# Optimization experiments

Hardware: AMD Instinct MI355X
Metric: run time of the kernel (lower is better)

The kernel has to match this reference:

```python
import jax, jax.numpy as jnp
import numpy as np

P_FACTOR = 3.0
EPS = 1e-12  # matches torch F.normalize clamp_min eps


def _normalize(x):
    # L2-normalize along the feature (last) axis, like F.normalize(x, dim=1) on 2D
    n = jnp.sqrt(jnp.sum(x * x, axis=-1, keepdims=True))
    return x / jnp.maximum(n, EPS)


def setup_inputs() -> dict:
    key = jax.random.key(0)
    ks = jax.random.split(key, 7)
    N, M, F, E = 8192, 16384, 768, 512
    X = jax.random.normal(ks[0], (N, F), dtype=jnp.float32)
    D = jax.random.normal(ks[1], (M, F), dtype=jnp.float32)
    r = jax.random.uniform(ks[2], (M, 1), dtype=jnp.float32)
    g_w = jax.random.normal(ks[3], (E, F), dtype=jnp.float32) * (1.0 / np.sqrt(F))
    g_b = jax.random.normal(ks[4], (E,), dtype=jnp.float32) * 0.01
    h_w = jax.random.normal(ks[5], (1, 1), dtype=jnp.float32)
    h_b = jax.random.normal(ks[6], (1,), dtype=jnp.float32) * 0.01
    return {"X": X, "D": D, "r": r, "g_w": g_w, "g_b": g_b, "h_w": h_w, "h_b": h_b}


def reference(X, D, r, g_w, g_b, h_w, h_b):
    # r = r * 2 - 1  (map [0,1] correctness labels to [-1,1])
    r2 = r * 2.0 - 1.0
    # g: shared linear embedding of queries and exemplars
    Xg = X @ g_w.T + g_b          # [N, E]
    Dg = D @ g_w.T + g_b          # [M, E]
    # Minerva: cosine similarity
    a = _normalize(Xg) @ _normalize(Dg).T   # [N, M]
    # power-sign activation: |a|^p * sign(a)
    a = jnp.power(jnp.abs(a), P_FACTOR) * jnp.sign(a)
    # echo = weighted sum of exemplar labels
    echo = a @ r2                 # [N, 1]
    # h: Linear(1,1) then sigmoid
    out = jax.nn.sigmoid(echo @ h_w.T + h_b)  # [N, 1]
    return out
```

## Files before the change

kernel.cpp:

```cpp
#include <hip/hip_runtime.h>
#include <stdint.h>

#define F_DIM 768
#define E_DIM 512

typedef __attribute__((ext_vector_type(4))) float f32x4;
typedef __attribute__((ext_vector_type(8))) __bf16 bf16x8;

__device__ __forceinline__ uint16_t f2bf(float f) {
  uint32_t u = __builtin_bit_cast(uint32_t, f);
  return (uint16_t)((u + 0x7FFFu + ((u >> 16) & 1u)) >> 16);
}

#define GLOAD_LDS16(g, l) __builtin_amdgcn_global_load_lds(                 \
    (const __attribute__((address_space(1))) void*)(g),                     \
    (__attribute__((address_space(3))) void*)(l), 16, 0, 0)

__global__ __launch_bounds__(256) void embed_gemm(
    const float* __restrict__ src, const float* __restrict__ gw,
    const float* __restrict__ gb, uint16_t* __restrict__ out) {
  __shared__ uint4 smem4[2048];
  char* smc = (char*)smem4;
  const int t = threadIdx.x;
  const int l = t & 63, w = t >> 6, wm = w >> 1, wn = w & 1;
  const int bx = blockIdx.x, by = blockIdx.y;
  const int g = l >> 4, x7 = l & 7;

  f32x4 acc[4][4];
#pragma unroll
  for (int a_ = 0; a_ < 4; ++a_)
#pragma unroll
    for (int b_ = 0; b_ < 4; ++b_) acc[a_][b_] = (f32x4){0.f, 0.f, 0.f, 0.f};

  const int rr0 = t >> 3;
  const int ss  = t & 7;

  for (int kk = 0; kk < F_DIM; kk += 64) {
    __syncthreads();
#pragma unroll
    for (int c = 0; c < 4; ++c) {
      const int rr = c * 32 + rr0;
      const int wb = rr * 128 + ((ss ^ (rr & 7)) << 4);
      {
        const float* p = src + (size_t)(bx * 128 + rr) * F_DIM + kk + ss * 8;
        float4 lo = *(const float4*)p;
        float4 hi = *(const float4*)(p + 4);
        uint4 pk;
        pk.x = f2bf(lo.x) | ((uint32_t)f2bf(lo.y) << 16);
        pk.y = f2bf(lo.z) | ((uint32_t)f2bf(lo.w) << 16);
        pk.z = f2bf(hi.x) | ((uint32_t)f2bf(hi.y) << 16);
        pk.w = f2bf(hi.z) | ((uint32_t)f2bf(hi.w) << 16);
        *(uint4*)(smc + wb) = pk;
      }
      {
        const float* p = gw + (size_t)(by * 128 + rr) * F_DIM + kk + ss * 8;
        float4 lo = *(const float4*)p;
        float4 hi = *(const float4*)(p + 4);
        uint4 pk;
        pk.x = f2bf(lo.x) | ((uint32_t)f2bf(lo.y) << 16);
        pk.y = f2bf(lo.z) | ((uint32_t)f2bf(lo.w) << 16);
        pk.z = f2bf(hi.x) | ((uint32_t)f2bf(hi.y) << 16);
        pk.w = f2bf(hi.z) | ((uint32_t)f2bf(hi.w) << 16);
        *(uint4*)(smc + 16384 + wb) = pk;
      }
    }
    __syncthreads();
#pragma unroll
    for (int ks = 0; ks < 2; ++ks) {
      const int slotoff = ((ks * 4 + g) ^ x7) << 4;
      bf16x8 af[4], bfr[4];
#pragma unroll
      for (int fm = 0; fm < 4; ++fm)
        af[fm] = *(const bf16x8*)(smc + (wm * 64 + fm * 16 + (l & 15)) * 128 + slotoff);
#pragma unroll
      for (int fn = 0; fn < 4; ++fn)
        bfr[fn] = *(const bf16x8*)(smc + 16384 + (wn * 64 + fn * 16 + (l & 15)) * 128 + slotoff);
#pragma unroll
      for (int fm = 0; fm < 4; ++fm)
#pragma unroll
        for (int fn = 0; fn < 4; ++fn)
          acc[fm][fn] = __builtin_amdgcn_mfma_f32_16x16x32_bf16(
              af[fm], bfr[fn], acc[fm][fn], 0, 0, 0);
    }
  }

  const int colb = by * 128 + wn * 64;
#pragma unroll
  for (int fn = 0; fn < 4; ++fn) {
    const int col = colb + fn * 16 + (l & 15);
    const float bias = gb[col];
#pragma unroll
    for (int fm = 0; fm < 4; ++fm) {
      const int rowb = bx * 128 + wm * 64 + fm * 16 + g * 4;
#pragma unroll
      for (int v = 0; v < 4; ++v)
        out[(size_t)(rowb + v) * E_DIM + col] = f2bf(acc[fm][fn][v] + bias);
    }
  }
}

__global__ __launch_bounds__(256) void l2norm_rows(uint16_t* __restrict__ eg) {
  const int row = blockIdx.x * 4 + (threadIdx.x >> 6);
  const int l = threadIdx.x & 63;
  uint16_t* p = eg + (size_t)row * E_DIM + l * 8;
  uint4 v = *(const uint4*)p;
  uint32_t wd[4] = {v.x, v.y, v.z, v.w};
  float f[8];
#pragma unroll
  for (int i = 0; i < 4; ++i) {
    f[2 * i]     = __builtin_bit_cast(float, (wd[i] & 0xFFFFu) << 16);
    f[2 * i + 1] = __builtin_bit_cast(float, wd[i] & 0xFFFF0000u);
  }
  float s = 0.f;
#pragma unroll
  for (int i = 0; i < 8; ++i) s += f[i] * f[i];
#pragma unroll
  for (int m = 1; m < 64; m <<= 1) s += __shfl_xor(s, m);
  const float inv = 1.0f / fmaxf(sqrtf(s), 1e-12f);
  uint4 o;
  o.x = f2bf(f[0] * inv) | ((uint32_t)f2bf(f[1] * inv) << 16);
  o.y = f2bf(f[2] * inv) | ((uint32_t)f2bf(f[3] * inv) << 16);
  o.z = f2bf(f[4] * inv) | ((uint32_t)f2bf(f[5] * inv) << 16);
  o.w = f2bf(f[6] * inv) | ((uint32_t)f2bf(f[7] * inv) << 16);
  *(uint4*)p = o;
}

__global__ __launch_bounds__(512, 2) void minerva_main256(
    const uint16_t* __restrict__ Xn, const uint16_t* __restrict__ Dn,
    const float* __restrict__ rin, float* __restrict__ echo) {
  extern __shared__ __align__(16) char smem[];
  const int t_ = threadIdx.x;
  const int l = t_ & 63, w = t_ >> 6;
  const int wm = w >> 2, wn = w & 3;
  const int bx = blockIdx.x, by = blockIdx.y;
  const int g = l >> 4, x7 = l & 7, l15 = l & 15;

  f32x4 acc[8][4];
#pragma unroll
  for (int a_ = 0; a_ < 8; ++a_)
#pragma unroll
    for (int b_ = 0; b_ < 4; ++b_) acc[a_][b_] = (f32x4){0.f, 0.f, 0.f, 0.f};

  const int rr = t_ >> 3, ss = t_ & 7;
  const int s0 = ss ^ (rr & 7);
  const uint16_t* gA = Xn + (size_t)(bx * 256 + rr) * E_DIM + s0 * 8;
  const uint16_t* gB = Dn + (size_t)(by * 256 + rr) * E_DIM + s0 * 8;
  char* ldsDst = smem + t_ * 16;

#define STG_A(CUR, KK, I) GLOAD_LDS16(gA + (size_t)(I) * 64 * E_DIM + (KK), \
                                      ldsDst + (CUR) * 32768 + (I) * 8192)
#define STG_B(CUR, KK, I) GLOAD_LDS16(gB + (size_t)(I) * 64 * E_DIM + (KK), \
                                      ldsDst + 65536 + (CUR) * 32768 + (I) * 8192)

#define PHASE(FM0, KS, READ_B, GL, LAST)                                       \
  {                                                                            \
    const int so = (((KS) * 4 + g) ^ x7) << 4;                                 \
    bf16x8 af[4];                                                              \
    _Pragma("unroll") for (int i_ = 0; i_ < 4; ++i_)                           \
        af[i_] = *(const bf16x8*)(bufA +                                       \
                  (wm * 128 + ((FM0) + i_) * 16 + l15) * 128 + so);            \
    if (READ_B) {                                                              \
      _Pragma("unroll") for (int j_ = 0; j_ < 4; ++j_)                         \
          bfr[j_] = *(const bf16x8*)(bufB +                                    \
                    (wn * 64 + j_ * 16 + l15) * 128 + so);                     \
    }                                                                          \
    GL;                                                                        \
    __builtin_amdgcn_s_barrier();                                              \
    __builtin_amdgcn_s_setprio(1);                                             \
    _Pragma("unroll") for (int i_ = 0; i_ < 4; ++i_)                           \
        _Pragma("unroll") for (int j_ = 0; j_ < 4; ++j_)                       \
            acc[(FM0) + i_][j_] = __builtin_amdgcn_mfma_f32_16x16x32_bf16(     \
                af[i_], bfr[j_], acc[(FM0) + i_][j_], 0, 0, 0);                \
    __builtin_amdgcn_s_setprio(0);                                             \
    if (LAST) asm volatile("s_waitcnt vmcnt(0)" ::: "memory");                 \
    __builtin_amdgcn_s_barrier();                                              \
  }

#define TILE(KKN, CUR, PF)                                                     \
  {                                                                            \
    char* bufA = smem + (CUR) * 32768;                                         \
    char* bufB = smem + 65536 + (CUR) * 32768;                                 \
    bf16x8 bfr[4];                                                             \
    PHASE(0, 0, 1, if (PF) { STG_A(1 - (CUR), KKN, 0); STG_A(1 - (CUR), KKN, 1); }, 0) \
    PHASE(4, 0, 0, if (PF) { STG_A(1 - (CUR), KKN, 2); STG_A(1 - (CUR), KKN, 3); }, 0) \
    PHASE(0, 1, 1, if (PF) { STG_B(1 - (CUR), KKN, 0); STG_B(1 - (CUR), KKN, 1); }, 0) \
    PHASE(4, 1, 0, if (PF) { STG_B(1 - (CUR), KKN, 2); STG_B(1 - (CUR), KKN, 3); }, 1) \
  }

  STG_A(0, 0, 0); STG_A(0, 0, 1); STG_A(0, 0, 2); STG_A(0, 0, 3);
  STG_B(0, 0, 0); STG_B(0, 0, 1); STG_B(0, 0, 2); STG_B(0, 0, 3);
  asm volatile("s_waitcnt vmcnt(0)" ::: "memory");
  __builtin_amdgcn_s_barrier();

  for (int t2 = 0; t2 < 8; t2 += 2) {
    TILE((t2 + 1) * 64, 0, 1);
    const int pf2 = (t2 < 6);
    TILE((t2 + 2) * 64, 1, pf2);
  }

  const int jb = by * 256 + wn * 64;
  float r2[4];
#pragma unroll
  for (int fn = 0; fn < 4; ++fn)
    r2[fn] = rin[jb + fn * 16 + l15] * 2.0f - 1.0f;
  const int rowb = bx * 256 + wm * 128;
#pragma unroll
  for (int fm = 0; fm < 8; ++fm) {
#pragma unroll
    for (int v = 0; v < 4; ++v) {
      float sum = 0.f;
#pragma unroll
      for (int fn = 0; fn < 4; ++fn) {
        const float a = acc[fm][fn][v];
        sum += a * a * a * r2[fn];
      }
      sum += __shfl_xor(sum, 1);
      sum += __shfl_xor(sum, 2);
      sum += __shfl_xor(sum, 4);
      sum += __shfl_xor(sum, 8);
      if (l15 == 0)
        atomicAdd(&echo[rowb + fm * 16 + g * 4 + v], sum);
    }
  }
#undef STG_A
#undef STG_B
#undef PHASE
#undef TILE
}

__global__ __launch_bounds__(256) void head_sigmoid(
    const float* __restrict__ echo, const float* __restrict__ hw,
    const float* __restrict__ hb, float* __restrict__ out, int n) {
  const int i = blockIdx.x * 256 + threadIdx.x;
  if (i < n) {
    const float e = echo[i] * hw[0] + hb[0];
    out[i] = 1.0f / (1.0f + __expf(-e));
  }
}

extern "C" void kernel_launch(void* const* d_in, const int* in_sizes, int n_in,
                              void* d_out, int out_size, void* d_ws, size_t ws_size,
                              hipStream_t stream) {
  const float* X  = (const float*)d_in[0];
  const float* D  = (const float*)d_in[1];
  const float* r  = (const float*)d_in[2];
  const float* gw = (const float*)d_in[3];
  const float* gb = (const float*)d_in[4];
  const float* hw = (const float*)d_in[5];
  const float* hb = (const float*)d_in[6];
  float* out = (float*)d_out;
  const int N = in_sizes[0] / F_DIM;
  const int M = in_sizes[1] / F_DIM;

  uint16_t* Xn = (uint16_t*)d_ws;
  uint16_t* Dn = Xn + (size_t)N * E_DIM;
  float* echo = (float*)((char*)d_ws + (size_t)(N + M) * E_DIM * 2);

  hipMemsetAsync(echo, 0, (size_t)N * sizeof(float), stream);

  (void)hipFuncSetAttribute((const void*)minerva_main256,
                            hipFuncAttributeMaxDynamicSharedMemorySize, 131072);

  dim3 blk(256);
  embed_gemm<<<dim3(N / 128, E_DIM / 128), blk, 0, stream>>>(X, gw, gb, Xn);
  embed_gemm<<<dim3(M / 128, E_DIM / 128), blk, 0, stream>>>(D, gw, gb, Dn);
  l2norm_rows<<<(N + M) / 4, blk, 0, stream>>>(Xn);
  minerva_main256<<<dim3(N / 256, M / 256), dim3(512), 131072, stream>>>(Xn, Dn, r, echo);
  head_sigmoid<<<(N + 255) / 256, blk, 0, stream>>>(echo, hw, hb, out, N);
}
```

Before: 330.5 us.

## Pre-convert inputs to bf16, async-load embed GEMM, defer normalization to epilogue

Converts X, D and g_w to bf16 in separate passes into one concatenated buffer. The embedding GEMM then runs as a single launch that streams tiles straight into LDS with global_load_lds. This replaces the per-tile fp32 loading and conversion that was repeated for every output column block. The L2 normalization pass now computes only inverse row norms, and these are folded into the cosine-cube epilogue as ix^3 and id^3 factors instead of rewriting normalized embeddings. This adds extra passes over the input data, hardcodes the problem sizes, and runs the similarity GEMM on unnormalized bf16 values.

Result: slower. 370.5 us (+12.1%).

```diff
diff --git a/kernel.cpp b/kernel.cpp
--- a/kernel.cpp
+++ b/kernel.cpp
@@ -3,6 +3,9 @@
 
 #define F_DIM 768
 #define E_DIM 512
+#define N_ROWS 8192
+#define M_ROWS 16384
+#define T_ROWS (N_ROWS + M_ROWS)
 
 typedef __attribute__((ext_vector_type(4))) float f32x4;
 typedef __attribute__((ext_vector_type(8))) __bf16 bf16x8;
@@ -16,15 +19,31 @@
     (const __attribute__((address_space(1))) void*)(g),                     \
     (__attribute__((address_space(3))) void*)(l), 16, 0, 0)
 
-__global__ __launch_bounds__(256) void embed_gemm(
-    const float* __restrict__ src, const float* __restrict__ gw,
+__global__ __launch_bounds__(256) void cvt_f32_bf16(
+    const float* __restrict__ src, uint16_t* __restrict__ dst, int n8) {
+  int i = blockIdx.x * 256 + threadIdx.x;
+  const int stride = gridDim.x * 256;
+  for (; i < n8; i += stride) {
+    const float4 lo = *(const float4*)(src + (size_t)i * 8);
+    const float4 hi = *(const float4*)(src + (size_t)i * 8 + 4);
+    uint4 pk;
+    pk.x = f2bf(lo.x) | ((uint32_t)f2bf(lo.y) << 16);
+    pk.y = f2bf(lo.z) | ((uint32_t)f2bf(lo.w) << 16);
+    pk.z = f2bf(hi.x) | ((uint32_t)f2bf(hi.y) << 16);
+    pk.w = f2bf(hi.z) | ((uint32_t)f2bf(hi.w) << 16);
+    *(uint4*)(dst + (size_t)i * 8) = pk;
+  }
+}
+
+__global__ __launch_bounds__(256) void embed_gemm_bf(
+    const uint16_t* __restrict__ cat, const uint16_t* __restrict__ gwb,
     const float* __restrict__ gb, uint16_t* __restrict__ out) {
   __shared__ uint4 smem4[2048];
   char* smc = (char*)smem4;
   const int t = threadIdx.x;
   const int l = t & 63, w = t >> 6, wm = w >> 1, wn = w & 1;
   const int bx = blockIdx.x, by = blockIdx.y;
-  const int g = l >> 4, x7 = l & 7;
+  const int g = l >> 4, x7 = l & 7, l15 = l & 15;
 
   f32x4 acc[4][4];
 #pragma unroll
@@ -32,37 +51,19 @@
 #pragma unroll
     for (int b_ = 0; b_ < 4; ++b_) acc[a_][b_] = (f32x4){0.f, 0.f, 0.f, 0.f};
 
-  const int rr0 = t >> 3;
-  const int ss  = t & 7;
+  const int rr0 = t >> 3, ss = t & 7;
+  const int s0 = ss ^ (rr0 & 7);
+  const uint16_t* gA = cat + (size_t)(bx * 128 + rr0) * F_DIM + s0 * 8;
+  const uint16_t* gB = gwb + (size_t)(by * 128 + rr0) * F_DIM + s0 * 8;
+  char* ldsA = smc + t * 16;
+  char* ldsB = smc + 16384 + t * 16;
 
   for (int kk = 0; kk < F_DIM; kk += 64) {
     __syncthreads();
 #pragma unroll
-    for (int c = 0; c < 4; ++c) {
-      const int rr = c * 32 + rr0;
-      const int wb = rr * 128 + ((ss ^ (rr & 7)) << 4);
-      {
-        const float* p = src + (size_t)(bx * 128 + rr) * F_DIM + kk + ss * 8;
-        float4 lo = *(const float4*)p;
-        float4 hi = *(const float4*)(p + 4);
-        uint4 pk;
-        pk.x = f2bf(lo.x) | ((uint32_t)f2bf(lo.y) << 16);
-        pk.y = f2bf(lo.z) | ((uint32_t)f2bf(lo.w) << 16);
-        pk.z = f2bf(hi.x) | ((uint32_t)f2bf(hi.y) << 16);
-        pk.w = f2bf(hi.z) | ((uint32_t)f2bf(hi.w) << 16);
-        *(uint4*)(smc + wb) = pk;
-      }
-      {
-        const float* p = gw + (size_t)(by * 128 + rr) * F_DIM + kk + ss * 8;
-        float4 lo = *(const float4*)p;
-        float4 hi = *(const float4*)(p + 4);
-        uint4 pk;
-        pk.x = f2bf(lo.x) | ((uint32_t)f2bf(lo.y) << 16);
-        pk.y = f2bf(lo.z) | ((uint32_t)f2bf(lo.w) << 16);
-        pk.z = f2bf(hi.x) | ((uint32_t)f2bf(hi.y) << 16);
-        pk.w = f2bf(hi.z) | ((uint32_t)f2bf(hi.w) << 16);
-        *(uint4*)(smc + 16384 + wb) = pk;
-      }
+    for (int i = 0; i < 4; ++i) {
+      GLOAD_LDS16(gA + (size_t)i * 32 * F_DIM + kk, ldsA + i * 4096);
+      GLOAD_LDS16(gB + (size_t)i * 32 * F_DIM + kk, ldsB + i * 4096);
     }
     __syncthreads();
 #pragma unroll
@@ -71,10 +72,10 @@
       bf16x8 af[4], bfr[4];
 #pragma unroll
       for (int fm = 0; fm < 4; ++fm)
-        af[fm] = *(const bf16x8*)(smc + (wm * 64 + fm * 16 + (l & 15)) * 128 + slotoff);
+        af[fm] = *(const bf16x8*)(smc + (wm * 64 + fm * 16 + l15) * 128 + slotoff);
 #pragma unroll
       for (int fn = 0; fn < 4; ++fn)
-        bfr[fn] = *(const bf16x8*)(smc + 16384 + (wn * 64 + fn * 16 + (l & 15)) * 128 + slotoff);
+        bfr[fn] = *(const bf16x8*)(smc + 16384 + (wn * 64 + fn * 16 + l15) * 128 + slotoff);
 #pragma unroll
       for (int fm = 0; fm < 4; ++fm)
 #pragma unroll
@@ -87,7 +88,7 @@
   const int colb = by * 128 + wn * 64;
 #pragma unroll
   for (int fn = 0; fn < 4; ++fn) {
-    const int col = colb + fn * 16 + (l & 15);
+    const int col = colb + fn * 16 + l15;
     const float bias = gb[col];
 #pragma unroll
     for (int fm = 0; fm < 4; ++fm) {
@@ -99,36 +100,34 @@
   }
 }
 
-__global__ __launch_bounds__(256) void l2norm_rows(uint16_t* __restrict__ eg) {
+__global__ __launch_bounds__(256) void rownorm_inv(
+    const uint16_t* __restrict__ eg, float* __restrict__ invn) {
   const int row = blockIdx.x * 4 + (threadIdx.x >> 6);
   const int l = threadIdx.x & 63;
-  uint16_t* p = eg + (size_t)row * E_DIM + l * 8;
+  const uint16_t* p = eg + (size_t)row * E_DIM + l * 8;
   uint4 v = *(const uint4*)p;
   uint32_t wd[4] = {v.x, v.y, v.z, v.w};
-  float f[8];
+  float s = 0.f;
 #pragma unroll
   for (int i = 0; i < 4; ++i) {
-    f[2 * i]     = __builtin_bit_cast(float, (wd[i] & 0xFFFFu) << 16);
-    f[2 * i + 1] = __builtin_bit_cast(float, wd[i] & 0xFFFF0000u);
-  }
-  float s = 0.f;
-#pragma unroll
-  for (int i = 0; i < 8; ++i) s += f[i] * f[i];
+    float a = __builtin_bit_cast(float, (wd[i] & 0xFFFFu) << 16);
+    float b = __builtin_bit_cast(float, wd[i] & 0xFFFF0000u);
+    s += a * a + b * b;
+  }
 #pragma unroll
   for (int m = 1; m < 64; m <<= 1) s += __shfl_xor(s, m);
-  const float inv = 1.0f / fmaxf(sqrtf(s), 1e-12f);
-  uint4 o;
-  o.x = f2bf(f[0] * inv) | ((uint32_t)f2bf(f[1] * inv) << 16);
-  o.y = f2bf(f[2] * inv) | ((uint32_t)f2bf(f[3] * inv) << 16);
-  o.z = f2bf(f[4] * inv) | ((uint32_t)f2bf(f[5] * inv) << 16);
-  o.w = f2bf(f[6] * inv) | ((uint32_t)f2bf(f[7] * inv) << 16);
-  *(uint4*)p = o;
+  if (l == 0) invn[row] = 1.0f / fmaxf(sqrtf(s), 1e-12f);
 }
 
 __global__ __launch_bounds__(512, 2) void minerva_main256(
-    const uint16_t* __restrict__ Xn, const uint16_t* __restrict__ Dn,
+    const uint16_t* __restrict__ Eg, const float* __restrict__ invn,
     const float* __restrict__ rin, float* __restrict__ echo) {
   extern __shared__ __align__(16) char smem[];
+  const uint16_t* Xn = Eg;
+  const uint16_t* Dn = Eg + (size_t)N_ROWS * E_DIM;
+  const float* invx = invn;
+  const float* invd = invn + N_ROWS;
+
   const int t_ = threadIdx.x;
   const int l = t_ & 63, w = t_ >> 6;
   const int wm = w >> 2, wn = w & 3;
@@ -199,10 +198,14 @@
   }
 
   const int jb = by * 256 + wn * 64;
-  float r2[4];
-#pragma unroll
-  for (int fn = 0; fn < 4; ++fn)
-    r2[fn] = rin[jb + fn * 16 + l15] * 2.0f - 1.0f;
+  float c[4];
+#pragma unroll
+  for (int fn = 0; fn < 4; ++fn) {
+    const int col = jb + fn * 16 + l15;
+    const float id = invd[col];
+    const float r2 = rin[col] * 2.0f - 1.0f;
+    c[fn] = id * id * id * r2;
+  }
   const int rowb = bx * 256 + wm * 128;
 #pragma unroll
   for (int fm = 0; fm < 8; ++fm) {
@@ -212,14 +215,17 @@
 #pragma unroll
       for (int fn = 0; fn < 4; ++fn) {
         const float a = acc[fm][fn][v];
-        sum += a * a * a * r2[fn];
+        sum += a * a * a * c[fn];
       }
       sum += __shfl_xor(sum, 1);
       sum += __shfl_xor(sum, 2);
       sum += __shfl_xor(sum, 4);
       sum += __shfl_xor(sum, 8);
-      if (l15 == 0)
-        atomicAdd(&echo[rowb + fm * 16 + g * 4 + v], sum);
+      if (l15 == 0) {
+        const int row = rowb + fm * 16 + g * 4 + v;
+        const float ix = invx[row];
+        atomicAdd(&echo[row], sum * ix * ix * ix);
+      }
     }
   }
 #undef STG_A
@@ -249,22 +255,28 @@
   const float* hw = (const float*)d_in[5];
   const float* hb = (const float*)d_in[6];
   float* out = (float*)d_out;
-  const int N = in_sizes[0] / F_DIM;
-  const int M = in_sizes[1] / F_DIM;
-
-  uint16_t* Xn = (uint16_t*)d_ws;
-  uint16_t* Dn = Xn + (size_t)N * E_DIM;
-  float* echo = (float*)((char*)d_ws + (size_t)(N + M) * E_DIM * 2);
-
-  hipMemsetAsync(echo, 0, (size_t)N * sizeof(float), stream);
+
+  uint16_t* cat  = (uint16_t*)d_ws;
+  uint16_t* gwb  = cat + (size_t)T_ROWS * F_DIM;
+  uint16_t* Eg   = gwb + (size_t)E_DIM * F_DIM;
+  float*    invn = (float*)(Eg + (size_t)T_ROWS * E_DIM);
+  float*    echo = invn + T_ROWS;
+
+  hipMemsetAsync(echo, 0, (size_t)N_ROWS * sizeof(float), stream);
 
   (void)hipFuncSetAttribute((const void*)minerva_main256,
                             hipFuncAttributeMaxDynamicSharedMemorySize, 131072);
 
   dim3 blk(256);
-  embed_gemm<<<dim3(N / 128, E_DIM / 128), blk, 0, stream>>>(X, gw, gb, Xn);
-  embed_gemm<<<dim3(M / 128, E_DIM / 128), blk, 0, stream>>>(D, gw, gb, Dn);
-  l2norm_rows<<<(N + M) / 4, blk, 0, stream>>>(Xn);
-  minerva_main256<<<dim3(N / 256, M / 256), dim3(512), 131072, stream>>>(Xn, Dn, r, echo);
-  head_sigmoid<<<(N + 255) / 256, blk, 0, stream>>>(echo, hw, hb, out, N);
-}
+  cvt_f32_bf16<<<2048, blk, 0, stream>>>(X, cat, N_ROWS * F_DIM / 8);
+  cvt_f32_bf16<<<2048, blk, 0, stream>>>(D, cat + (size_t)N_ROWS * F_DIM,
+                                         M_ROWS * F_DIM / 8);
+  cvt_f32_bf16<<<192, blk, 0, stream>>>(gw, gwb, E_DIM * F_DIM / 8);
+
+  embed_gemm_bf<<<dim3(T_ROWS / 128, E_DIM / 128), blk, 0, stream>>>(cat, gwb, gb, Eg);
+  rownorm_inv<<<T_ROWS / 4, blk, 0, stream>>>(Eg, invn);
+
+  minerva_main256<<<dim3(N_ROWS / 256, M_ROWS / 256), dim3(512), 131072, stream>>>(
+      Eg, invn, r, echo);
+  head_sigmoid<<<(N_ROWS + 255) / 256, blk, 0, stream>>>(echo, hw, hb, out, N_ROWS);
+}
```
